# Optimization experiments

Hardware: AMD Instinct MI355X
Metric: run time of the kernel (lower is better)

The kernel has to match this reference:

```python
import jax, jax.numpy as jnp
import numpy as np

B, N, L, C, K = 2, 8192, 8192, 128, 8
RADIUS = 0.4

def _gather(t, idx):
    # t: [B,L,D], idx: [B,N,K] -> [B,N,K,D]
    b, n, k = idx.shape
    return jnp.take_along_axis(t, idx.reshape(b, n * k)[:, :, None], axis=1).reshape(b, n, k, t.shape[-1])

def _ln(x, g, b):
    m = x.mean(-1, keepdims=True)
    v = x.var(-1, keepdims=True)
    return (x - m) * jax.lax.rsqrt(v + 1e-5) * g + b

def setup_inputs() -> dict:
    key = jax.random.key(0)
    ks = jax.random.split(key, 16)
    F = 4 * C
    def w(k, i, o):
        return jax.random.normal(k, (i, o), jnp.float32) / np.sqrt(i).astype(np.float32)
    return {
        "q_xyz": jax.random.uniform(ks[0], (B, N, 3), jnp.float32),
        "q_feat": jax.random.normal(ks[1], (B, N, C), jnp.float32),
        "kv_xyz": jax.random.uniform(ks[2], (B, L, 3), jnp.float32),
        "kv_feat": jax.random.normal(ks[3], (B, L, C), jnp.float32),
        "kv_pad": jnp.zeros((B, L), bool),
        "pos_w1": w(ks[4], 3, C), "pos_b1": jnp.zeros((C,), jnp.float32),
        "pos_w2": w(ks[5], C, C), "pos_b2": jnp.zeros((C,), jnp.float32),
        "attn_w": w(ks[6], C, C), "attn_b": jnp.zeros((C,), jnp.float32),
        "lin_w": w(ks[7], C, C),
        "lin_src_w": w(ks[8], C, C),
        "lin_dst_w": w(ks[9], C, C),
        "ln1_g": jnp.ones((C,), jnp.float32), "ln1_b": jnp.zeros((C,), jnp.float32),
        "ffn_w1": w(ks[10], C, F), "ffn_b1": jnp.zeros((F,), jnp.float32),
        "ffn_w2": w(ks[11], F, C), "ffn_b2": jnp.zeros((C,), jnp.float32),
        "ln2_g": jnp.ones((C,), jnp.float32), "ln2_b": jnp.zeros((C,), jnp.float32),
    }

def reference(q_xyz, q_feat, kv_xyz, kv_feat, kv_pad,
              pos_w1, pos_b1, pos_w2, pos_b2, attn_w, attn_b,
              lin_w, lin_src_w, lin_dst_w, ln1_g, ln1_b,
              ffn_w1, ffn_b1, ffn_w2, ffn_b2, ln2_g, ln2_b):
    # --- radius graph: up to K nearest kv points within RADIUS per query ---
    d2 = jnp.sum((q_xyz[:, :, None, :] - kv_xyz[:, None, :, :]) ** 2, -1)  # [B,N,L]
    ok = (d2 <= RADIUS ** 2) & (~kv_pad)[:, None, :]
    neg_d2, idx = jax.lax.top_k(jnp.where(ok, -d2, -jnp.inf), K)  # [B,N,K]
    ev = jnp.isfinite(neg_d2)  # edge-valid mask [B,N,K]

    # --- PointTransformerConv (vector attention, per-edge) ---
    pos_j = _gather(kv_xyz, idx)                           # [B,N,K,3]
    rel = q_xyz[:, :, None, :] - pos_j                     # pos_i - pos_j
    # pos_nn: MLP([3,C,C], plain_last=False) => ReLU after each Linear
    delta = jax.nn.relu(jax.nn.relu(rel @ pos_w1 + pos_b1) @ pos_w2 + pos_b2)  # [B,N,K,C]
    a_src = _gather(kv_feat @ lin_src_w, idx)              # [B,N,K,C]
    a_dst = q_feat @ lin_dst_w                             # [B,N,C]
    x_j = _gather(kv_feat @ lin_w, idx)                    # [B,N,K,C]
    # attn_nn: MLP([C,C], plain_last=False) => Linear + ReLU
    alpha = jax.nn.relu((a_dst[:, :, None, :] - a_src + delta) @ attn_w + attn_b)
    # segment softmax over the K neighbors (invalid edges masked out)
    scores = jnp.where(ev[..., None], alpha, -jnp.inf)
    mx = jnp.max(scores, axis=2, keepdims=True)
    mx = jnp.where(jnp.isfinite(mx), mx, 0.0)
    e = jnp.where(ev[..., None], jnp.exp(scores - mx), 0.0)
    attn = e / jnp.maximum(e.sum(2, keepdims=True), 1e-12)
    agg = jnp.sum(attn * (x_j + delta), axis=2)            # [B,N,C]

    # --- residual + LN + FFN + LN (dropout = identity at eval) ---
    out = _ln(q_feat + agg, ln1_g, ln1_b)
    h = jax.nn.gelu(out @ ffn_w1 + ffn_b1, approximate=False) @ ffn_w2 + ffn_b2
    return _ln(out + h, ln2_g, ln2_b)
```

## Files before the change

kernel.cpp:

```cpp
#include <hip/hip_runtime.h>
#include <math.h>

#define NB 2
#define NQ 8192
#define NL 8192
#define NC 128
#define NKN 8
#define NF 512
#define MQ (NB*NQ)

typedef __attribute__((ext_vector_type(8))) short bf16x8;
typedef __attribute__((ext_vector_type(4))) float f32x4;

__device__ __forceinline__ unsigned short f2bf_u(float f){
    unsigned u = __float_as_uint(f);
    return (unsigned short)((u + 0x7FFFu + ((u>>16)&1u)) >> 16);
}
__device__ __forceinline__ float bf2f(unsigned short s){
    return __uint_as_float(((unsigned)s) << 16);
}


__global__ __launch_bounds__(256) void grid_zero_kernel(int* __restrict__ p)
{
    int t = blockIdx.x*256 + threadIdx.x;
    p[t] = 0;
}

__device__ __forceinline__ int cell_coord(float x) {
    int c = (int)(x * 16.0f);
    return min(15, max(0, c));
}

__global__ __launch_bounds__(256) void grid_count_kernel(
    const float* __restrict__ kxyz, const unsigned char* __restrict__ pad,
    int* __restrict__ cnt)
{
    int t = blockIdx.x*256 + threadIdx.x;
    if (pad[t]) return;
    int bat = t >> 13;
    float x = kxyz[t*3+0], y = kxyz[t*3+1], z = kxyz[t*3+2];
    int cell = (cell_coord(z)*16 + cell_coord(y))*16 + cell_coord(x);
    atomicAdd(&cnt[bat*4096 + cell], 1);
}

__global__ __launch_bounds__(1024) void grid_scan_kernel(
    const int* __restrict__ cnt, int* __restrict__ cs)
{
    __shared__ int wsum[17];
    int t = threadIdx.x;
    int v[8]; int s = 0;
    #pragma unroll
    for (int k = 0; k < 8; ++k) { v[k] = s; s += cnt[t*8 + k]; }
    int lane = t & 63, w = t >> 6;
    int inc = s;
    #pragma unroll
    for (int d = 1; d < 64; d <<= 1) {
        int o = __shfl_up(inc, d);
        if (lane >= d) inc += o;
    }
    if (lane == 63) wsum[w] = inc;
    __syncthreads();
    if (t == 0) {
        int a = 0;
        for (int i = 0; i < 16; ++i) { int x = wsum[i]; wsum[i] = a; a += x; }
        wsum[16] = a;
    }
    __syncthreads();
    int base = wsum[w] + (inc - s);
    #pragma unroll
    for (int k = 0; k < 8; ++k) cs[t*8 + k] = base + v[k];
    if (t == 1023) cs[8192] = wsum[16];
}

__global__ __launch_bounds__(256) void grid_scatter_kernel(
    const float* __restrict__ kxyz, const unsigned char* __restrict__ pad,
    const int* __restrict__ cs, int* __restrict__ fill, float4* __restrict__ ro)
{
    int t = blockIdx.x*256 + threadIdx.x;
    if (pad[t]) return;
    int bat = t >> 13, i = t & 8191;
    float x = kxyz[t*3+0], y = kxyz[t*3+1], z = kxyz[t*3+2];
    int cell = bat*4096 + (cell_coord(z)*16 + cell_coord(y))*16 + cell_coord(x);
    int pos = cs[cell] + atomicAdd(&fill[cell], 1);
    ro[pos] = make_float4(x, y, z, __int_as_float(i));
}

__device__ __forceinline__ void insert8(float cd, int id, float dk[8], int ik[8]) {
    if (cd < dk[7]) {
        dk[7] = cd; ik[7] = id;
        #pragma unroll
        for (int r = 6; r >= 0; --r) {
            bool sw = dk[r+1] < dk[r];
            float td = dk[r]; int ti = ik[r];
            dk[r]   = sw ? dk[r+1] : dk[r];
            ik[r]   = sw ? ik[r+1] : ik[r];
            dk[r+1] = sw ? td : dk[r+1];
            ik[r+1] = sw ? ti : ik[r+1];
        }
    }
}

template<int W>
__device__ __forceinline__ void scan_block(int l, int cx, int cy, int cz,
    float qx, float qy, float qz, const int* __restrict__ CS,
    const float4* __restrict__ RO, float dk[8], int ik[8])
{
    const int D = 2*W + 1;
    int xs = max(0, cx - W), xe = min(15, cx + W);
    int nx = xe - xs + 1;
    for (int r = l; r < D*D; r += 8) {
        int dz = r / D - W, dy = r % D - W;
        int zz = cz + dz, yy = cy + dy;
        if ((unsigned)zz > 15u || (unsigned)yy > 15u) continue;
        int c0 = (zz*16 + yy)*16 + xs;
        int s = CS[c0], e = CS[c0 + nx];
        for (int p = s; p < e; ++p) {
            float4 v = RO[p];
            float dx = qx - v.x, dyv = qy - v.y, dzv = qz - v.z;
            float cd = dx*dx + dyv*dyv + dzv*dzv;
            insert8(cd, __float_as_int(v.w), dk, ik);
        }
    }
}

__device__ __forceinline__ void merge8(float dk[8], int ik[8]) {
    #pragma unroll
    for (int m = 1; m <= 4; m <<= 1) {
        float od[8]; int oi[8];
        #pragma unroll
        for (int r = 0; r < 8; ++r) {
            od[r] = __shfl_xor(dk[r], m);
            oi[r] = __shfl_xor(ik[r], m);
        }
        float nd[8]; int ni[8];
        #pragma unroll
        for (int r = 0; r < 8; ++r) {
            bool take = od[7-r] < dk[r];
            nd[r] = take ? od[7-r] : dk[r];
            ni[r] = take ? oi[7-r] : ik[r];
        }
        #pragma unroll
        for (int st = 4; st >= 1; st >>= 1) {
            #pragma unroll
            for (int r = 0; r < 8; ++r) {
                if ((r & st) == 0 && (r | st) < 8) {
                    int b = r | st;
                    bool sw = nd[b] < nd[r];
                    float td = nd[r]; int ti = ni[r];
                    nd[r] = sw ? nd[b] : nd[r];
                    ni[r] = sw ? ni[b] : ni[r];
                    nd[b] = sw ? td : nd[b];
                    ni[b] = sw ? ti : ni[b];
                }
            }
        }
        #pragma unroll
        for (int r = 0; r < 8; ++r) { dk[r] = nd[r]; ik[r] = ni[r]; }
    }
}

__global__ __launch_bounds__(256) void radius_grid_query_kernel(
    const float* __restrict__ qxyz, const int* __restrict__ cellstart,
    const float4* __restrict__ reorder, int* __restrict__ idxout)
{
    const int tid  = threadIdx.x;
    const int l    = tid & 7;
    const int qloc = tid >> 3;
    const int gq   = blockIdx.x*32 + qloc;
    const int bat  = gq >> 13;
    const float qx = qxyz[gq*3+0], qy = qxyz[gq*3+1], qz = qxyz[gq*3+2];
    const int cx = cell_coord(qx), cy = cell_coord(qy), cz = cell_coord(qz);
    const int* CS = cellstart + bat*4096;
    const float R2  = (float)(0.4*0.4);
    const float R2P = __uint_as_float(__float_as_uint(R2) + 1u);

    float dk[8]; int ik[8];
    #pragma unroll
    for (int r = 0; r < 8; ++r) { dk[r] = R2P; ik[r] = -1; }

    scan_block<2>(l, cx, cy, cz, qx, qy, qz, CS, reorder, dk, ik);
    merge8(dk, ik);
    bool done = dk[7] <= 0.015625f;

    if (!done) {
        #pragma unroll
        for (int r = 0; r < 8; ++r) { dk[r] = R2P; ik[r] = -1; }
        scan_block<4>(l, cx, cy, cz, qx, qy, qz, CS, reorder, dk, ik);
        merge8(dk, ik);
        done = dk[7] <= 0.0625f;
    }
    if (!done) {
        #pragma unroll
        for (int r = 0; r < 8; ++r) { dk[r] = R2P; ik[r] = -1; }
        scan_block<16>(l, cx, cy, cz, qx, qy, qz, CS, reorder, dk, ik);
        merge8(dk, ik);
    }

    if (l == 0) {
        int o[8];
        #pragma unroll
        for (int r = 0; r < 8; ++r) o[r] = (dk[r] <= R2) ? ik[r] : -1;
        int4 a = {o[0], o[1], o[2], o[3]};
        int4 b = {o[4], o[5], o[6], o[7]};
        *(int4*)&idxout[(size_t)gq*8 + 0] = a;
        *(int4*)&idxout[(size_t)gq*8 + 4] = b;
    }
}

__global__ __launch_bounds__(256) void wprep_kernel(
    const float* __restrict__ wA, const float* __restrict__ wB,
    unsigned short* __restrict__ imgA, unsigned short* __restrict__ imgB)
{
    int t = blockIdx.x*256 + threadIdx.x;
    int k = t >> 7, c = t & 127;
    int off = (k >> 5)*5120 + c*40 + (k & 31);
    imgA[off] = f2bf_u(wA[t]);
    imgB[off] = f2bf_u(wB[t]);
}

__global__ __launch_bounds__(256) void wprep2_kernel(
    const float* __restrict__ W, unsigned short* __restrict__ img, int lgN)
{
    int t = blockIdx.x*256 + threadIdx.x;
    int k = t >> lgN, n = t & ((1 << lgN) - 1);
    int Nd = 1 << lgN;
    img[(((k >> 5)*Nd + n) << 5) + (k & 31)] = f2bf_u(W[t]);
}

__device__ inline float gelu_exact(float x) {
    return 0.5f*x*(1.0f + erff(x*0.7071067811865476f));
}

template<int ACT, bool OUTBF>
__global__ __launch_bounds__(256) void gemm_mfma(
    const float* __restrict__ A, const unsigned short* __restrict__ Bimg,
    const float* __restrict__ bias, void* __restrict__ outv,
    int Kd, int Nd)
{
    __shared__ unsigned short sA[64*32];
    __shared__ unsigned short sB[128*32];
    const int tid = threadIdx.x;
    const int w = tid >> 6, lane = tid & 63, l15 = lane & 15, quad = lane >> 4;
    const int row0 = blockIdx.x*64, col0 = blockIdx.y*128;

    f32x4 acc[8];
    #pragma unroll
    for (int t=0;t<8;t++){ acc[t][0]=0.f; acc[t][1]=0.f; acc[t][2]=0.f; acc[t][3]=0.f; }

    const int nch = Kd >> 5;
    for (int kc = 0; kc < nch; ++kc) {
        __syncthreads();
        #pragma unroll
        for (int it = 0; it < 2; ++it) {
            int idx = it*256 + tid;
            int r = idx >> 3, kq = idx & 7;
            float4 a4 = *(const float4*)&A[(size_t)(row0+r)*Kd + kc*32 + kq*4];
            ushort4 pk = { f2bf_u(a4.x), f2bf_u(a4.y), f2bf_u(a4.z), f2bf_u(a4.w) };
            *(ushort4*)&sA[r*32 + kq*4] = pk;
        }
        const int4* bsrc = (const int4*)(Bimg + ((size_t)kc*Nd + col0)*32);
        #pragma unroll
        for (int it = 0; it < 2; ++it) {
            int o = it*256 + tid;
            ((int4*)sB)[o] = bsrc[o];
        }
        __syncthreads();
        bf16x8 af = *(const bf16x8*)&sA[(w*16 + l15)*32 + quad*8];
        #pragma unroll
        for (int t = 0; t < 8; ++t) {
            bf16x8 bf = *(const bf16x8*)&sB[(16*t + l15)*32 + quad*8];
            acc[t] = __builtin_amdgcn_mfma_f32_16x16x32_bf16(af, bf, acc[t], 0, 0, 0);
        }
    }

    const int rowb = row0 + w*16 + quad*4;
    #pragma unroll
    for (int t = 0; t < 8; ++t) {
        int col = col0 + 16*t + l15;
        float bv = bias ? bias[col] : 0.f;
        #pragma unroll
        for (int r = 0; r < 4; ++r) {
            float x = acc[t][r] + bv;
            if (ACT == 1) x = gelu_exact(x);
            if (OUTBF) ((unsigned short*)outv)[(size_t)(rowb+r)*Nd + col] = f2bf_u(x);
            else       ((float*)outv)[(size_t)(rowb+r)*Nd + col] = x;
        }
    }
}

__global__ __launch_bounds__(256) void gemm2_ln_mfma(
    const unsigned short* __restrict__ Abf, const unsigned short* __restrict__ Bimg,
    const float* __restrict__ b2, const float* __restrict__ res,
    const float* __restrict__ g, const float* __restrict__ bb,
    float* __restrict__ out)
{
    __shared__ unsigned short sA[64*32];
    __shared__ unsigned short sB[128*32];
    const int tid = threadIdx.x;
    const int w = tid >> 6, lane = tid & 63, l15 = lane & 15, quad = lane >> 4;
    const int row0 = blockIdx.x*64;

    f32x4 acc[8];
    #pragma unroll
    for (int t=0;t<8;t++){ acc[t][0]=0.f; acc[t][1]=0.f; acc[t][2]=0.f; acc[t][3]=0.f; }

    for (int kc = 0; kc < 16; ++kc) {
        __syncthreads();
        {
            int r = tid >> 2, kq = tid & 3;
            ((int4*)sA)[tid] = *(const int4*)&Abf[(size_t)(row0+r)*NF + kc*32 + kq*8];
        }
        const int4* bsrc = (const int4*)(Bimg + (size_t)kc*NC*32);
        #pragma unroll
        for (int it = 0; it < 2; ++it) {
            int o = it*256 + tid;
            ((int4*)sB)[o] = bsrc[o];
        }
        __syncthreads();
        bf16x8 af = *(const bf16x8*)&sA[(w*16 + l15)*32 + quad*8];
        #pragma unroll
        for (int t = 0; t < 8; ++t) {
            bf16x8 bf = *(const bf16x8*)&sB[(16*t + l15)*32 + quad*8];
            acc[t] = __builtin_amdgcn_mfma_f32_16x16x32_bf16(af, bf, acc[t], 0, 0, 0);
        }
    }

    const int rowb = row0 + w*16 + quad*4;
    #pragma unroll
    for (int r = 0; r < 4; ++r) {
        int row = rowb + r;
        float xv[8]; float S = 0.f;
        #pragma unroll
        for (int t = 0; t < 8; ++t) {
            int col = 16*t + l15;
            xv[t] = acc[t][r] + b2[col] + res[(size_t)row*NC + col];
            S += xv[t];
        }
        #pragma unroll
        for (int m = 1; m <= 8; m <<= 1) S += __shfl_xor(S, m);
        float mean = S * (1.f/128.f);
        float V = 0.f;
        #pragma unroll
        for (int t = 0; t < 8; ++t) { float d = xv[t]-mean; V += d*d; }
        #pragma unroll
        for (int m = 1; m <= 8; m <<= 1) V += __shfl_xor(V, m);
        float rstd = rsqrtf(V*(1.f/128.f) + 1e-5f);
        #pragma unroll
        for (int t = 0; t < 8; ++t) {
            int col = 16*t + l15;
            out[(size_t)row*NC + col] = (xv[t]-mean)*rstd*g[col] + bb[col];
        }
    }
}

__global__ __launch_bounds__(256) void attn_mfma_kernel(
    const float* __restrict__ qxyz, const float* __restrict__ qfeat,
    const float* __restrict__ kxyz,
    const float* __restrict__ posw1, const float* __restrict__ posb1,
    const float* __restrict__ posb2, const float* __restrict__ attnb,
    const float* __restrict__ ln1g, const float* __restrict__ ln1b,
    const unsigned short* __restrict__ wimg1, const unsigned short* __restrict__ wimg2,
    const int* __restrict__ idx, const unsigned short* __restrict__ vfeat,
    const unsigned short* __restrict__ sfeat, const float* __restrict__ adst,
    float* __restrict__ out1)
{
    __shared__ int4 s_wc[640];
    __shared__ int4 s_t4[1088];
    __shared__ float s_w1[384];
    __shared__ float s_b1[128], s_b2[128], s_ab[128], s_g[128], s_bb[128];
    __shared__ int   s_j[64];

    const int tid  = threadIdx.x;
    const int w    = tid >> 6;
    const int lane = tid & 63;
    const int l15  = lane & 15;
    const int quad = lane >> 4;
    const int qbase = blockIdx.x*8 + w*2;
    const int bat  = (blockIdx.x*8) >> 13;

    if (tid < 128) {
        s_b1[tid] = posb1[tid]; s_b2[tid] = posb2[tid];
        s_ab[tid] = attnb[tid]; s_g[tid] = ln1g[tid]; s_bb[tid] = ln1b[tid];
    } else {
        int i = tid - 128;
        s_w1[i] = posw1[i]; s_w1[128+i] = posw1[128+i]; s_w1[256+i] = posw1[256+i];
    }
    if (tid < 64) s_j[tid] = idx[(size_t)blockIdx.x*64 + tid];
    __syncthreads();

    bf16x8 h1f[4];
    {
        int e  = w*16 + l15;
        int qh = qbase + (l15 >> 3);
        int j  = s_j[e];
        int jc = j < 0 ? 0 : j;
        const float* kp = kxyz + ((size_t)(bat*NL + jc))*3;
        float rx = qxyz[qh*3+0]-kp[0], ry = qxyz[qh*3+1]-kp[1], rz = qxyz[qh*3+2]-kp[2];
        #pragma unroll
        for (int kk=0;kk<4;kk++){
            #pragma unroll
            for (int jj=0;jj<8;jj++){
                int c = kk*32 + quad*8 + jj;
                float h = s_b1[c] + rx*s_w1[c] + ry*s_w1[128+c] + rz*s_w1[256+c];
                h = fmaxf(h, 0.f);
                h1f[kk][jj] = (short)f2bf_u(h);
            }
        }
    }

    f32x4 acc[8];
    #pragma unroll
    for (int t=0;t<8;t++){ acc[t][0]=0.f; acc[t][1]=0.f; acc[t][2]=0.f; acc[t][3]=0.f; }

    for (int kk=0;kk<4;kk++){
        __syncthreads();
        const int4* src = (const int4*)(wimg1 + (size_t)kk*5120);
        #pragma unroll
        for (int r=0;r<3;r++){
            int o = r*256 + tid;
            if (o < 640) s_wc[o] = src[o];
        }
        __syncthreads();
        const char* wb = (const char*)s_wc;
        #pragma unroll
        for (int t=0;t<8;t++){
            bf16x8 wf = *(const bf16x8*)(wb + (16*t + l15)*80 + quad*16);
            acc[t] = __builtin_amdgcn_mfma_f32_16x16x32_bf16(h1f[kk], wf, acc[t], 0, 0, 0);
        }
    }

    f32x4 dreg[8];
    #pragma unroll
    for (int t=0;t<8;t++){
        float b2v = s_b2[16*t + l15];
        #pragma unroll
        for (int r=0;r<4;r++) dreg[t][r] = fmaxf(acc[t][r] + b2v, 0.f);
    }

    int jr[4]; bool val[4];
    #pragma unroll
    for (int r=0;r<4;r++){
        int j = s_j[w*16 + quad*4 + r];
        val[r] = (j >= 0); jr[r] = j < 0 ? 0 : j;
    }
    const int qt = qbase + (quad >> 1);
    char* st = (char*)s_t4 + w*4352;
    #pragma unroll
    for (int t=0;t<8;t++){
        float ad = adst[(size_t)qt*NC + 16*t + l15];
        #pragma unroll
        for (int r=0;r<4;r++){
            float sv = bf2f(sfeat[((size_t)(bat*NL + jr[r]))*NC + 16*t + l15]);
            float tv = ad - sv + dreg[t][r];
            *(unsigned short*)(st + (quad*4+r)*272 + (16*t+l15)*2) = f2bf_u(tv);
        }
    }

    f32x4 acc2[8];
    #pragma unroll
    for (int t=0;t<8;t++){ acc2[t][0]=0.f; acc2[t][1]=0.f; acc2[t][2]=0.f; acc2[t][3]=0.f; }

    for (int kk=0;kk<4;kk++){
        __syncthreads();
        const int4* src = (const int4*)(wimg2 + (size_t)kk*5120);
        #pragma unroll
        for (int r=0;r<3;r++){
            int o = r*256 + tid;
            if (o < 640) s_wc[o] = src[o];
        }
        __syncthreads();
        bf16x8 tf = *(const bf16x8*)(st + l15*272 + kk*64 + quad*16);
        const char* wb = (const char*)s_wc;
        #pragma unroll
        for (int t=0;t<8;t++){
            bf16x8 wf = *(const bf16x8*)(wb + (16*t + l15)*80 + quad*16);
            acc2[t] = __builtin_amdgcn_mfma_f32_16x16x32_bf16(tf, wf, acc2[t], 0, 0, 0);
        }
    }

    float ex[8][4]; float dnm[8];
    #pragma unroll
    for (int t=0;t<8;t++){
        float ab = s_ab[16*t + l15];
        float s0 = val[0] ? fmaxf(acc2[t][0] + ab, 0.f) : -INFINITY;
        float s1 = val[1] ? fmaxf(acc2[t][1] + ab, 0.f) : -INFINITY;
        float s2 = val[2] ? fmaxf(acc2[t][2] + ab, 0.f) : -INFINITY;
        float s3 = val[3] ? fmaxf(acc2[t][3] + ab, 0.f) : -INFINITY;
        float mx = fmaxf(fmaxf(s0,s1), fmaxf(s2,s3));
        mx = fmaxf(mx, __shfl_xor(mx, 16));
        if (mx < -1e37f) mx = 0.f;
        ex[t][0] = __expf(s0 - mx);
        ex[t][1] = __expf(s1 - mx);
        ex[t][2] = __expf(s2 - mx);
        ex[t][3] = __expf(s3 - mx);
        float sm = ex[t][0]+ex[t][1]+ex[t][2]+ex[t][3];
        sm += __shfl_xor(sm, 16);
        dnm[t] = fmaxf(sm, 1e-12f);
    }

    float part[8];
    #pragma unroll
    for (int t=0;t<8;t++){
        float p = 0.f;
        #pragma unroll
        for (int r=0;r<4;r++){
            float vv = bf2f(vfeat[((size_t)(bat*NL + jr[r]))*NC + 16*t + l15]);
            p += ex[t][r] * (vv + dreg[t][r]);
        }
        p += __shfl_xor(p, 16);
        part[t] = p / dnm[t];
    }

    float xln[8];
    float S = 0.f;
    #pragma unroll
    for (int t=0;t<8;t++){
        xln[t] = qfeat[(size_t)qt*NC + 16*t + l15] + part[t];
        S += xln[t];
    }
    #pragma unroll
    for (int m=1;m<=8;m<<=1) S += __shfl_xor(S, m);
    float mean = S * (1.f/128.f);
    float V = 0.f;
    #pragma unroll
    for (int t=0;t<8;t++){ float d = xln[t]-mean; V += d*d; }
    #pragma unroll
    for (int m=1;m<=8;m<<=1) V += __shfl_xor(V, m);
    float rstd = rsqrtf(V*(1.f/128.f) + 1e-5f);

    if ((quad & 1) == 0){
        #pragma unroll
        for (int t=0;t<8;t++){
            int c = 16*t + l15;
            out1[(size_t)qt*NC + c] = (xln[t]-mean)*rstd*s_g[c] + s_bb[c];
        }
    }
}

extern "C" void kernel_launch(void* const* d_in, const int* in_sizes, int n_in,
                              void* d_out, int out_size, void* d_ws, size_t ws_size,
                              hipStream_t stream)
{
    (void)in_sizes; (void)n_in; (void)out_size; (void)ws_size;
    const float* q_xyz   = (const float*)d_in[0];
    const float* q_feat  = (const float*)d_in[1];
    const float* kv_xyz  = (const float*)d_in[2];
    const float* kv_feat = (const float*)d_in[3];
    const unsigned char* kv_pad = (const unsigned char*)d_in[4];
    const float* pos_w1  = (const float*)d_in[5];
    const float* pos_b1  = (const float*)d_in[6];
    const float* pos_w2  = (const float*)d_in[7];
    const float* pos_b2  = (const float*)d_in[8];
    const float* attn_w  = (const float*)d_in[9];
    const float* attn_b  = (const float*)d_in[10];
    const float* lin_w   = (const float*)d_in[11];
    const float* lin_src_w = (const float*)d_in[12];
    const float* lin_dst_w = (const float*)d_in[13];
    const float* ln1_g   = (const float*)d_in[14];
    const float* ln1_b   = (const float*)d_in[15];
    const float* ffn_w1  = (const float*)d_in[16];
    const float* ffn_b1  = (const float*)d_in[17];
    const float* ffn_w2  = (const float*)d_in[18];
    const float* ffn_b2  = (const float*)d_in[19];
    const float* ln2_g   = (const float*)d_in[20];
    const float* ln2_b   = (const float*)d_in[21];

    float* ws    = (float*)d_ws;
    int*   idx   = (int*)d_ws;
    unsigned short* vfeat = (unsigned short*)(ws + 131072);
    unsigned short* sfeat = (unsigned short*)(ws + 131072 + 2097152);
    float* adst  = ws + 131072 + 2*2097152;
    float* out1  = adst + 2097152;
    float* Hreg  = out1 + 2097152;
    unsigned short* Hbuf = (unsigned short*)Hreg;

    float4* reorder  = (float4*)Hreg;
    int* cellcnt   = (int*)(reorder + 16384);
    int* cellfill  = cellcnt + 8192;
    int* cellstart = cellfill + 8192;

    unsigned short* imgb = (unsigned short*)((char*)Hreg + 18u*1024*1024);
    unsigned short* wimg1 = imgb;
    unsigned short* wimg2 = imgb + 20480;
    unsigned short* wv    = imgb + 40960;
    unsigned short* wsr   = imgb + 57344;
    unsigned short* wd    = imgb + 73728;
    unsigned short* wf1   = imgb + 90112;
    unsigned short* wf2   = imgb + 155648;

    wprep_kernel<<<dim3(64), dim3(256), 0, stream>>>(pos_w2, attn_w, wimg1, wimg2);
    wprep2_kernel<<<dim3(64),  dim3(256), 0, stream>>>(lin_w,     wv,  7);
    wprep2_kernel<<<dim3(64),  dim3(256), 0, stream>>>(lin_src_w, wsr, 7);
    wprep2_kernel<<<dim3(64),  dim3(256), 0, stream>>>(lin_dst_w, wd,  7);
    wprep2_kernel<<<dim3(256), dim3(256), 0, stream>>>(ffn_w1,    wf1, 9);
    wprep2_kernel<<<dim3(256), dim3(256), 0, stream>>>(ffn_w2,    wf2, 7);

    grid_zero_kernel<<<dim3(64), dim3(256), 0, stream>>>(cellcnt);
    grid_count_kernel<<<dim3(64), dim3(256), 0, stream>>>(kv_xyz, kv_pad, cellcnt);
    grid_scan_kernel<<<dim3(1), dim3(1024), 0, stream>>>(cellcnt, cellstart);
    grid_scatter_kernel<<<dim3(64), dim3(256), 0, stream>>>(kv_xyz, kv_pad, cellstart, cellfill, reorder);
    radius_grid_query_kernel<<<dim3(MQ/32), dim3(256), 0, stream>>>(q_xyz, cellstart, reorder, idx);

    gemm_mfma<0,true ><<<dim3(MQ/64,1), dim3(256), 0, stream>>>(kv_feat, wv,  nullptr, vfeat, 128, 128);
    gemm_mfma<0,true ><<<dim3(MQ/64,1), dim3(256), 0, stream>>>(kv_feat, wsr, nullptr, sfeat, 128, 128);
    gemm_mfma<0,false><<<dim3(MQ/64,1), dim3(256), 0, stream>>>(q_feat,  wd,  nullptr, adst,  128, 128);

    attn_mfma_kernel<<<dim3(MQ/8), dim3(256), 0, stream>>>(
        q_xyz, q_feat, kv_xyz,
        pos_w1, pos_b1, pos_b2, attn_b, ln1_g, ln1_b,
        wimg1, wimg2, idx, vfeat, sfeat, adst, out1);

    gemm_mfma<1,true ><<<dim3(MQ/64,4), dim3(256), 0, stream>>>(out1, wf1, ffn_b1, Hbuf, 128, 512);
    gemm2_ln_mfma<<<dim3(MQ/64), dim3(256), 0, stream>>>(Hbuf, wf2, ffn_b2, out1, ln2_g, ln2_b, (float*)d_out);
}
```

Before: 260.4 us.

## Fuse weight prep, merge V/S projections, stage whole weights in LDS

Replaces six weight-conversion launches with one prep kernel and merges the lin_w and lin_src_w GEMMs into a single 256-wide output, so each gathered neighbor row holds both V and S features contiguously. In the attention kernel the full 128x128 bf16 weight matrices are loaded into LDS once per stage instead of in four chunks with paired barriers. Neighbor V/S rows are gathered into LDS with vectorized int4 loads rather than scattered scalar bf16 reads. This cuts launches, barriers and uncoalesced gather traffic, at the cost of a larger LDS footprint (32KB weights plus V/T tiles) that may reduce occupancy. The unpadded weight layout may also introduce LDS bank conflicts.

```diff
diff --git a/kernel.cpp b/kernel.cpp
--- a/kernel.cpp
+++ b/kernel.cpp
@@ -208,24 +208,39 @@
     }
 }
 
-__global__ __launch_bounds__(256) void wprep_kernel(
-    const float* __restrict__ wA, const float* __restrict__ wB,
-    unsigned short* __restrict__ imgA, unsigned short* __restrict__ imgB)
+__global__ __launch_bounds__(256) void prep_all_kernel(
+    const float* __restrict__ posw2, const float* __restrict__ attnw,
+    const float* __restrict__ lin_w, const float* __restrict__ lin_src_w,
+    const float* __restrict__ lin_dst_w,
+    const float* __restrict__ ffn_w1, const float* __restrict__ ffn_w2,
+    unsigned short* __restrict__ imgb)
 {
     int t = blockIdx.x*256 + threadIdx.x;
-    int k = t >> 7, c = t & 127;
-    int off = (k >> 5)*5120 + c*40 + (k & 31);
-    imgA[off] = f2bf_u(wA[t]);
-    imgB[off] = f2bf_u(wB[t]);
-}
-
-__global__ __launch_bounds__(256) void wprep2_kernel(
-    const float* __restrict__ W, unsigned short* __restrict__ img, int lgN)
-{
-    int t = blockIdx.x*256 + threadIdx.x;
-    int k = t >> lgN, n = t & ((1 << lgN) - 1);
-    int Nd = 1 << lgN;
-    img[(((k >> 5)*Nd + n) << 5) + (k & 31)] = f2bf_u(W[t]);
+    if (t < 16384) {
+        int k = t >> 7, n = t & 127;
+        imgb[(k >> 5)*4096 + n*32 + (k & 31)] = f2bf_u(posw2[t]);
+    } else if (t < 32768) {
+        int u = t - 16384;
+        int k = u >> 7, n = u & 127;
+        imgb[16384 + (k >> 5)*4096 + n*32 + (k & 31)] = f2bf_u(attnw[u]);
+    } else if (t < 65536) {
+        int u = t - 32768;
+        int k = u >> 8, n = u & 255;
+        float v = (n < 128) ? lin_w[k*128 + n] : lin_src_w[k*128 + (n-128)];
+        imgb[32768 + ((k >> 5)*256 + n)*32 + (k & 31)] = f2bf_u(v);
+    } else if (t < 81920) {
+        int u = t - 65536;
+        int k = u >> 7, n = u & 127;
+        imgb[65536 + ((k >> 5)*128 + n)*32 + (k & 31)] = f2bf_u(lin_dst_w[u]);
+    } else if (t < 147456) {
+        int u = t - 81920;
+        int k = u >> 9, n = u & 511;
+        imgb[81920 + ((k >> 5)*512 + n)*32 + (k & 31)] = f2bf_u(ffn_w1[u]);
+    } else {
+        int u = t - 147456;
+        int k = u >> 7, n = u & 127;
+        imgb[147456 + ((k >> 5)*128 + n)*32 + (k & 31)] = f2bf_u(ffn_w2[u]);
+    }
 }
 
 __device__ inline float gelu_exact(float x) {
@@ -361,12 +376,12 @@
     const float* __restrict__ posb2, const float* __restrict__ attnb,
     const float* __restrict__ ln1g, const float* __restrict__ ln1b,
     const unsigned short* __restrict__ wimg1, const unsigned short* __restrict__ wimg2,
-    const int* __restrict__ idx, const unsigned short* __restrict__ vfeat,
-    const unsigned short* __restrict__ sfeat, const float* __restrict__ adst,
-    float* __restrict__ out1)
-{
-    __shared__ int4 s_wc[640];
-    __shared__ int4 s_t4[1088];
+    const int* __restrict__ idx, const unsigned short* __restrict__ vs,
+    const float* __restrict__ adst, float* __restrict__ out1)
+{
+    __shared__ unsigned short s_w[16384];
+    __shared__ unsigned short s_V[4*16*136];
+    __shared__ unsigned short s_T[4*16*136];
     __shared__ float s_w1[384];
     __shared__ float s_b1[128], s_b2[128], s_ab[128], s_g[128], s_bb[128];
     __shared__ int   s_j[64];
@@ -387,7 +402,22 @@
         s_w1[i] = posw1[i]; s_w1[128+i] = posw1[128+i]; s_w1[256+i] = posw1[256+i];
     }
     if (tid < 64) s_j[tid] = idx[(size_t)blockIdx.x*64 + tid];
+    #pragma unroll
+    for (int r = 0; r < 8; ++r)
+        ((int4*)s_w)[r*256 + tid] = ((const int4*)wimg1)[r*256 + tid];
     __syncthreads();
+
+    #pragma unroll
+    for (int i = 0; i < 4; ++i) {
+        int ix = lane + i*64;
+        int el = ix >> 4, c16 = ix & 15;
+        int j = s_j[w*16 + el];
+        int jc = j < 0 ? 0 : j;
+        const int4* rp = (const int4*)(vs + ((size_t)(bat*NL + jc))*256);
+        int dst = (w*16 + el)*136 + c16*8;
+        *(int4*)&s_V[dst] = rp[c16];
+        *(int4*)&s_T[dst] = rp[16 + c16];
+    }
 
     bf16x8 h1f[4];
     {
@@ -412,20 +442,11 @@
     f32x4 acc[8];
     #pragma unroll
     for (int t=0;t<8;t++){ acc[t][0]=0.f; acc[t][1]=0.f; acc[t][2]=0.f; acc[t][3]=0.f; }
-
+    #pragma unroll
     for (int kk=0;kk<4;kk++){
-        __syncthreads();
-        const int4* src = (const int4*)(wimg1 + (size_t)kk*5120);
-        #pragma unroll
-        for (int r=0;r<3;r++){
-            int o = r*256 + tid;
-            if (o < 640) s_wc[o] = src[o];
-        }
-        __syncthreads();
-        const char* wb = (const char*)s_wc;
         #pragma unroll
         for (int t=0;t<8;t++){
-            bf16x8 wf = *(const bf16x8*)(wb + (16*t + l15)*80 + quad*16);
+            bf16x8 wf = *(const bf16x8*)&s_w[kk*4096 + (16*t + l15)*32 + quad*8];
             acc[t] = __builtin_amdgcn_mfma_f32_16x16x32_bf16(h1f[kk], wf, acc[t], 0, 0, 0);
         }
     }
@@ -445,37 +466,43 @@
         val[r] = (j >= 0); jr[r] = j < 0 ? 0 : j;
     }
     const int qt = qbase + (quad >> 1);
-    char* st = (char*)s_t4 + w*4352;
-    #pragma unroll
-    for (int t=0;t<8;t++){
-        float ad = adst[(size_t)qt*NC + 16*t + l15];
-        #pragma unroll
-        for (int r=0;r<4;r++){
-            float sv = bf2f(sfeat[((size_t)(bat*NL + jr[r]))*NC + 16*t + l15]);
-            float tv = ad - sv + dreg[t][r];
-            *(unsigned short*)(st + (quad*4+r)*272 + (16*t+l15)*2) = f2bf_u(tv);
-        }
-    }
+    float ad[8];
+    #pragma unroll
+    for (int t=0;t<8;t++) ad[t] = adst[(size_t)qt*NC + 16*t + l15];
+
+    __syncthreads();
+
+    #pragma unroll
+    for (int r = 0; r < 8; ++r)
+        ((int4*)s_w)[r*256 + tid] = ((const int4*)wimg2)[r*256 + tid];
+
+    {
+        unsigned short* st = s_T + w*16*136;
+        #pragma unroll
+        for (int t=0;t<8;t++){
+            #pragma unroll
+            for (int r=0;r<4;r++){
+                int o = (quad*4 + r)*136 + 16*t + l15;
+                float sv = bf2f(st[o]);
+                st[o] = f2bf_u(ad[t] - sv + dreg[t][r]);
+            }
+        }
+    }
+    __syncthreads();
 
     f32x4 acc2[8];
     #pragma unroll
     for (int t=0;t<8;t++){ acc2[t][0]=0.f; acc2[t][1]=0.f; acc2[t][2]=0.f; acc2[t][3]=0.f; }
-
-    for (int kk=0;kk<4;kk++){
-        __syncthreads();
-        const int4* src = (const int4*)(wimg2 + (size_t)kk*5120);
-        #pragma unroll
-        for (int r=0;r<3;r++){
-            int o = r*256 + tid;
-            if (o < 640) s_wc[o] = src[o];
-        }
-        __syncthreads();
-        bf16x8 tf = *(const bf16x8*)(st + l15*272 + kk*64 + quad*16);
-        const char* wb = (const char*)s_wc;
-        #pragma unroll
-        for (int t=0;t<8;t++){
-            bf16x8 wf = *(const bf16x8*)(wb + (16*t + l15)*80 + quad*16);
-            acc2[t] = __builtin_amdgcn_mfma_f32_16x16x32_bf16(tf, wf, acc2[t], 0, 0, 0);
+    {
+        const unsigned short* st = s_T + w*16*136;
+        #pragma unroll
+        for (int kk=0;kk<4;kk++){
+            bf16x8 tf = *(const bf16x8*)&st[l15*136 + kk*32 + quad*8];
+            #pragma unroll
+            for (int t=0;t<8;t++){
+                bf16x8 wf = *(const bf16x8*)&s_w[kk*4096 + (16*t + l15)*32 + quad*8];
+                acc2[t] = __builtin_amdgcn_mfma_f32_16x16x32_bf16(tf, wf, acc2[t], 0, 0, 0);
+            }
         }
     }
 
@@ -505,7 +532,7 @@
         float p = 0.f;
         #pragma unroll
         for (int r=0;r<4;r++){
-            float vv = bf2f(vfeat[((size_t)(bat*NL + jr[r]))*NC + 16*t + l15]);
+            float vv = bf2f(s_V[(w*16 + quad*4 + r)*136 + 16*t + l15]);
             p += ex[t][r] * (vv + dreg[t][r]);
         }
         p += __shfl_xor(p, 16);
@@ -568,8 +595,7 @@
 
     float* ws    = (float*)d_ws;
     int*   idx   = (int*)d_ws;
-    unsigned short* vfeat = (unsigned short*)(ws + 131072);
-    unsigned short* sfeat = (unsigned short*)(ws + 131072 + 2097152);
+    unsigned short* vs = (unsigned short*)(ws + 131072);
     float* adst  = ws + 131072 + 2*2097152;
     float* out1  = adst + 2097152;
     float* Hreg  = out1 + 2097152;
@@ -580,21 +606,16 @@
     int* cellfill  = cellcnt + 8192;
     int* cellstart = cellfill + 8192;
 
-    unsigned short* imgb = (unsigned short*)((char*)Hreg + 18u*1024*1024);
+    unsigned short* imgb  = (unsigned short*)((char*)Hreg + 18u*1024*1024);
     unsigned short* wimg1 = imgb;
-    unsigned short* wimg2 = imgb + 20480;
-    unsigned short* wv    = imgb + 40960;
-    unsigned short* wsr   = imgb + 57344;
-    unsigned short* wd    = imgb + 73728;
-    unsigned short* wf1   = imgb + 90112;
-    unsigned short* wf2   = imgb + 155648;
-
-    wprep_kernel<<<dim3(64), dim3(256), 0, stream>>>(pos_w2, attn_w, wimg1, wimg2);
-    wprep2_kernel<<<dim3(64),  dim3(256), 0, stream>>>(lin_w,     wv,  7);
-    wprep2_kernel<<<dim3(64),  dim3(256), 0, stream>>>(lin_src_w, wsr, 7);
-    wprep2_kernel<<<dim3(64),  dim3(256), 0, stream>>>(lin_dst_w, wd,  7);
-    wprep2_kernel<<<dim3(256), dim3(256), 0, stream>>>(ffn_w1,    wf1, 9);
-    wprep2_kernel<<<dim3(256), dim3(256), 0, stream>>>(ffn_w2,    wf2, 7);
+    unsigned short* wimg2 = imgb + 16384;
+    unsigned short* wvs   = imgb + 32768;
+    unsigned short* wd    = imgb + 65536;
+    unsigned short* wf1   = imgb + 81920;
+    unsigned short* wf2   = imgb + 147456;
+
+    prep_all_kernel<<<dim3(832), dim3(256), 0, stream>>>(
+        pos_w2, attn_w, lin_w, lin_src_w, lin_dst_w, ffn_w1, ffn_w2, imgb);
 
     grid_zero_kernel<<<dim3(64), dim3(256), 0, stream>>>(cellcnt);
     grid_count_kernel<<<dim3(64), dim3(256), 0, stream>>>(kv_xyz, kv_pad, cellcnt);
@@ -602,14 +623,13 @@
     grid_scatter_kernel<<<dim3(64), dim3(256), 0, stream>>>(kv_xyz, kv_pad, cellstart, cellfill, reorder);
     radius_grid_query_kernel<<<dim3(MQ/32), dim3(256), 0, stream>>>(q_xyz, cellstart, reorder, idx);
 
-    gemm_mfma<0,true ><<<dim3(MQ/64,1), dim3(256), 0, stream>>>(kv_feat, wv,  nullptr, vfeat, 128, 128);
-    gemm_mfma<0,true ><<<dim3(MQ/64,1), dim3(256), 0, stream>>>(kv_feat, wsr, nullptr, sfeat, 128, 128);
-    gemm_mfma<0,false><<<dim3(MQ/64,1), dim3(256), 0, stream>>>(q_feat,  wd,  nullptr, adst,  128, 128);
+    gemm_mfma<0,true ><<<dim3(MQ/64,2), dim3(256), 0, stream>>>(kv_feat, wvs, nullptr, vs,   128, 256);
+    gemm_mfma<0,false><<<dim3(MQ/64,1), dim3(256), 0, stream>>>(q_feat,  wd,  nullptr, adst, 128, 128);
 
     attn_mfma_kernel<<<dim3(MQ/8), dim3(256), 0, stream>>>(
         q_xyz, q_feat, kv_xyz,
         pos_w1, pos_b1, pos_b2, attn_b, ln1_g, ln1_b,
-        wimg1, wimg2, idx, vfeat, sfeat, adst, out1);
+        wimg1, wimg2, idx, vs, adst, out1);
 
     gemm_mfma<1,true ><<<dim3(MQ/64,4), dim3(256), 0, stream>>>(out1, wf1, ffn_b1, Hbuf, 128, 512);
     gemm2_ln_mfma<<<dim3(MQ/64), dim3(256), 0, stream>>>(Hbuf, wf2, ffn_b2, out1, ln2_g, ln2_b, (float*)d_out);
```

Result: faster. 234.2 us (-10.1%).
